# Kernel tuning notes

Hardware: AMD Instinct MI355X
Metric: run time of the kernel (lower is better)

The kernel has to match this reference:

```python
import jax, jax.numpy as jnp
import numpy as np

HEADS = 8
ALPHA = 0.2  # leaky relu negative slope


def setup_inputs() -> dict:
    key = jax.random.key(0)
    k1, k2, k3 = jax.random.split(key, 3)
    B, S, IN, H, F = 8, 1024, 768, HEADS, 64
    node_features = jax.random.normal(k1, (B, S, IN), dtype=jnp.float32)
    attention_mask = jnp.ones((B, S), dtype=jnp.int32)
    W = jax.random.normal(k2, (IN, H * F), dtype=jnp.float32) * 0.02
    a = jax.random.normal(k3, (2 * F,), dtype=jnp.float32) * 0.02
    return {"node_features": node_features, "attention_mask": attention_mask, "W": W, "a": a}


def reference(node_features, attention_mask, W, a):
    B, S, _ = node_features.shape
    H = HEADS
    F = W.shape[1] // H
    # Wh: [B, S, H, F]
    Wh = (node_features @ W).reshape(B, S, H, F)
    # Additive score a([Wh_i || Wh_j]) decomposes exactly into src_i + dst_j
    a_src, a_dst = a[:F], a[F:]
    src = jnp.einsum('bshf,f->bsh', Wh, a_src)  # contribution of node i
    dst = jnp.einsum('bshf,f->bsh', Wh, a_dst)  # contribution of node j
    e = src[:, :, None, :] + dst[:, None, :, :]          # [B, i, j, H]
    e = jax.nn.leaky_relu(e, negative_slope=ALPHA)
    e = jnp.transpose(e, (0, 3, 1, 2))                   # [B, H, i, j]
    mask = attention_mask[:, None, None, :] == 0         # mask over j
    e = jnp.where(mask, -jnp.inf, e)
    attn = jax.nn.softmax(e, axis=-1)                    # [B, H, S, S]
    # weighted sum over neighbors j: [B, i, H, F]
    h_prime = jnp.einsum('bhij,bjhf->bihf', attn, Wh)
    return h_prime.reshape(B, S, H * F)
```

## Files before the change

kernel.cpp:

```cpp
#include <hip/hip_runtime.h>
#include <math.h>


typedef __attribute__((ext_vector_type(8))) short short8;
typedef __attribute__((ext_vector_type(4))) float floatx4;

union Frag { short8 s8; uint4 u4; };

__device__ inline unsigned as_u(float f) { union { float f; unsigned u; } v; v.f = f; return v.u; }
__device__ inline float as_f(unsigned u) { union { unsigned u; float f; } v; v.u = u; return v.f; }

__device__ inline unsigned pk_rne(float a, float b) {
  unsigned ua = as_u(a); ua = ua + 0x7fffu + ((ua >> 16) & 1u);
  unsigned ub = as_u(b); ub = ub + 0x7fffu + ((ub >> 16) & 1u);
  return (ua >> 16) | (ub & 0xffff0000u);
}
__device__ inline unsigned short f2bf(float f) {
  unsigned u = as_u(f); u = u + 0x7fffu + ((u >> 16) & 1u);
  return (unsigned short)(u >> 16);
}

__global__ __launch_bounds__(256) void conv_w(const float* __restrict__ W,
                                              unsigned short* __restrict__ WbT) {
  __shared__ unsigned short tile[64][72];
  int kt = blockIdx.x >> 3, nt = blockIdx.x & 7;
  int k0 = kt * 64, n0 = nt * 64;
  int t = threadIdx.x;
  int kr = t >> 2, cs = (t & 3) * 16;
#pragma unroll
  for (int q = 0; q < 4; q++) {
    float4 v = *(const float4*)&W[(k0 + kr) * 512 + n0 + cs + q * 4];
    tile[cs + q * 4 + 0][kr] = f2bf(v.x);
    tile[cs + q * 4 + 1][kr] = f2bf(v.y);
    tile[cs + q * 4 + 2][kr] = f2bf(v.z);
    tile[cs + q * 4 + 3][kr] = f2bf(v.w);
  }
  __syncthreads();
  int nr = t >> 2, ks = (t & 3) * 16;
  uint4 d0 = *(const uint4*)&tile[nr][ks];
  uint4 d1 = *(const uint4*)&tile[nr][ks + 8];
  *(uint4*)&WbT[(n0 + nr) * 768 + k0 + ks] = d0;
  *(uint4*)&WbT[(n0 + nr) * 768 + k0 + ks + 8] = d1;
}

__global__ __launch_bounds__(256) void xconv(const float* __restrict__ X,
                                             unsigned short* __restrict__ Xb) {
  const int total = 8192 * 768 / 8;
  int stride = gridDim.x * 256;
  for (int i = blockIdx.x * 256 + threadIdx.x; i < total; i += stride) {
    float4 v0 = *(const float4*)&X[i * 8];
    float4 v1 = *(const float4*)&X[i * 8 + 4];
    uint4 o;
    o.x = pk_rne(v0.x, v0.y); o.y = pk_rne(v0.z, v0.w);
    o.z = pk_rne(v1.x, v1.y); o.w = pk_rne(v1.z, v1.w);
    *(uint4*)&Xb[i * 8] = o;
  }
}

__global__ __launch_bounds__(256) void gemm_xw(const unsigned short* __restrict__ Xb,
                                               const unsigned short* __restrict__ WbT,
                                               const float* __restrict__ a,
                                               const int* __restrict__ mask,
                                               unsigned short* __restrict__ WhT,
                                               float* __restrict__ srcT,
                                               float* __restrict__ dstT) {
  __shared__ unsigned short Asm[2][64 * 64];
  __shared__ unsigned short Bsm[2][64 * 64];
  __shared__ float sd[2][64], dd[2][64];
  int t = threadIdx.x, w = t >> 6, lane = t & 63;
  int quad = lane >> 4, l15 = lane & 15;
  int m0 = blockIdx.x * 64, n0 = blockIdx.y * 64;
  int wm = (w & 1) * 32, wn = (w >> 1) * 32;

  floatx4 acc[2][2];
#pragma unroll
  for (int mt = 0; mt < 2; mt++)
#pragma unroll
    for (int nt = 0; nt < 2; nt++)
#pragma unroll
      for (int r = 0; r < 4; r++) acc[mt][nt][r] = 0.f;

  int sf = t >> 3, skb = t & 7;
  int swz = (skb ^ (sf & 7)) * 8;
  const unsigned short* ga0 = &Xb[(m0 + sf) * 768 + skb * 8];
  const unsigned short* ga1 = &Xb[(m0 + sf + 32) * 768 + skb * 8];
  const unsigned short* gb0 = &WbT[(n0 + sf) * 768 + skb * 8];
  const unsigned short* gb1 = &WbT[(n0 + sf + 32) * 768 + skb * 8];

  int rdA0 = (wm + l15) * 64, rdA1 = (wm + 16 + l15) * 64;
  int keyA0 = (wm + l15) & 7, keyA1 = (wm + 16 + l15) & 7;
  int rdB0 = (wn + l15) * 64, rdB1 = (wn + 16 + l15) * 64;
  int keyB0 = (wn + l15) & 7, keyB1 = (wn + 16 + l15) & 7;

  uint4 av0 = *(const uint4*)&ga0[0];
  uint4 av1 = *(const uint4*)&ga1[0];
  uint4 bv0 = *(const uint4*)&gb0[0];
  uint4 bv1 = *(const uint4*)&gb1[0];

#pragma unroll 2
  for (int kc = 0; kc < 12; kc++) {
    unsigned short* bufA = &Asm[kc & 1][0];
    unsigned short* bufB = &Bsm[kc & 1][0];
    *(uint4*)&bufA[sf * 64 + swz] = av0;
    *(uint4*)&bufA[(sf + 32) * 64 + swz] = av1;
    *(uint4*)&bufB[sf * 64 + swz] = bv0;
    *(uint4*)&bufB[(sf + 32) * 64 + swz] = bv1;
    __syncthreads();
    if (kc < 11) {
      int off = (kc + 1) * 64;
      av0 = *(const uint4*)&ga0[off];
      av1 = *(const uint4*)&ga1[off];
      bv0 = *(const uint4*)&gb0[off];
      bv1 = *(const uint4*)&gb1[off];
    }
#pragma unroll
    for (int kc2 = 0; kc2 < 2; kc2++) {
      int kb = kc2 * 4 + quad;
      Frag fa0 = *(const Frag*)&bufA[rdA0 + ((kb ^ keyA0) * 8)];
      Frag fa1 = *(const Frag*)&bufA[rdA1 + ((kb ^ keyA1) * 8)];
      Frag fb0 = *(const Frag*)&bufB[rdB0 + ((kb ^ keyB0) * 8)];
      Frag fb1 = *(const Frag*)&bufB[rdB1 + ((kb ^ keyB1) * 8)];
      acc[0][0] = __builtin_amdgcn_mfma_f32_16x16x32_bf16(fa0.s8, fb0.s8, acc[0][0], 0, 0, 0);
      acc[0][1] = __builtin_amdgcn_mfma_f32_16x16x32_bf16(fa0.s8, fb1.s8, acc[0][1], 0, 0, 0);
      acc[1][0] = __builtin_amdgcn_mfma_f32_16x16x32_bf16(fa1.s8, fb0.s8, acc[1][0], 0, 0, 0);
      acc[1][1] = __builtin_amdgcn_mfma_f32_16x16x32_bf16(fa1.s8, fb1.s8, acc[1][1], 0, 0, 0);
    }
  }
  int h = n0 >> 6;
#pragma unroll
  for (int mt = 0; mt < 2; mt++) {
#pragma unroll
    for (int nt = 0; nt < 2; nt++) {
      int f = (wn + nt * 16 + l15) & 63;
      int m = m0 + wm + mt * 16 + quad * 4;
      int b = m >> 10, s = m & 1023;
      floatx4 cc = acc[mt][nt];
      uint2 st;
      st.x = pk_rne(cc[0], cc[1]);
      st.y = pk_rne(cc[2], cc[3]);
      *(uint2*)&WhT[((b * 8 + h) * 64 + f) * 1024 + s] = st;
    }
  }
  {
    float asv[2] = {a[wn + l15], a[wn + 16 + l15]};
    float adv[2] = {a[64 + wn + l15], a[64 + wn + 16 + l15]};
    float psrc[2][4], pdst[2][4];
#pragma unroll
    for (int mt = 0; mt < 2; mt++)
#pragma unroll
      for (int r = 0; r < 4; r++) {
        psrc[mt][r] = acc[mt][0][r] * asv[0] + acc[mt][1][r] * asv[1];
        pdst[mt][r] = acc[mt][0][r] * adv[0] + acc[mt][1][r] * adv[1];
      }
#pragma unroll
    for (int off = 1; off < 16; off <<= 1)
#pragma unroll
      for (int mt = 0; mt < 2; mt++)
#pragma unroll
        for (int r = 0; r < 4; r++) {
          psrc[mt][r] += __shfl_xor(psrc[mt][r], off);
          pdst[mt][r] += __shfl_xor(pdst[mt][r], off);
        }
    __syncthreads();
    if (l15 == 0) {
      int half = w >> 1;
#pragma unroll
      for (int mt = 0; mt < 2; mt++)
#pragma unroll
        for (int r = 0; r < 4; r++) {
          int m = wm + mt * 16 + quad * 4 + r;
          sd[half][m] = psrc[mt][r];
          dd[half][m] = pdst[mt][r];
        }
    }
    __syncthreads();
    if (t < 64) {
      int m = m0 + t;
      int b = m >> 10, s = m & 1023;
      float sv = sd[0][t] + sd[1][t];
      float dvv = dd[0][t] + dd[1][t];
      srcT[(b * 8 + h) * 1024 + s] = sv;
      dstT[(b * 8 + h) * 1024 + s] = mask[b * 1024 + s] ? dvv : -1e30f;
    }
  }
}

__global__ __launch_bounds__(256) void gat_attn(const unsigned short* __restrict__ WhT,
                                                const float* __restrict__ srcT,
                                                const float* __restrict__ dstT,
                                                float* __restrict__ out) {
  __shared__ unsigned short Bs[2][64 * 64];
  int t = threadIdx.x, w = t >> 6, lane = t & 63;
  int quad = lane >> 4, l15 = lane & 15;
  int bh = blockIdx.x, b = bh >> 3;
  int iw = blockIdx.y * 64 + w * 16;

  floatx4 acc[4], lacc;
#pragma unroll
  for (int ft = 0; ft < 4; ft++)
#pragma unroll
    for (int r = 0; r < 4; r++) acc[ft][r] = 0.f;
#pragma unroll
  for (int r = 0; r < 4; r++) lacc[r] = 0.f;

  float src_r = srcT[bh * 1024 + iw + l15];

  Frag ones;
  ones.u4.x = 0x3F803F80u; ones.u4.y = 0x3F803F80u;
  ones.u4.z = 0x3F803F80u; ones.u4.w = 0x3F803F80u;

  const unsigned short* Wg = WhT + bh * 64 * 1024;
  const float* dbase = &dstT[bh * 1024 + quad * 8];
  int sf0 = t >> 3, skb = t & 7;
  int swz = (skb ^ (sf0 & 7)) * 8;

  uint4 g0 = *(const uint4*)&Wg[sf0 * 1024 + skb * 8];
  uint4 g1 = *(const uint4*)&Wg[(sf0 + 32) * 1024 + skb * 8];
  float4 dv[4];
  dv[0] = *(const float4*)&dbase[0];
  dv[1] = *(const float4*)&dbase[4];
  dv[2] = *(const float4*)&dbase[32];
  dv[3] = *(const float4*)&dbase[36];

#pragma unroll 2
  for (int jt = 0; jt < 16; jt++) {
    int j0 = jt * 64;
    unsigned short* buf = &Bs[jt & 1][0];
    *(uint4*)&buf[sf0 * 64 + swz] = g0;
    *(uint4*)&buf[(sf0 + 32) * 64 + swz] = g1;
    __syncthreads();
    float4 ndv[4] = {dv[0], dv[1], dv[2], dv[3]};
    if (jt < 15) {
      g0 = *(const uint4*)&Wg[sf0 * 1024 + j0 + 64 + skb * 8];
      g1 = *(const uint4*)&Wg[(sf0 + 32) * 1024 + j0 + 64 + skb * 8];
      ndv[0] = *(const float4*)&dbase[j0 + 64];
      ndv[1] = *(const float4*)&dbase[j0 + 68];
      ndv[2] = *(const float4*)&dbase[j0 + 96];
      ndv[3] = *(const float4*)&dbase[j0 + 100];
    }
    Frag fragA[2];
#pragma unroll
    for (int jc = 0; jc < 2; jc++) {
      float dj[8] = {dv[jc * 2].x, dv[jc * 2].y, dv[jc * 2].z, dv[jc * 2].w,
                     dv[jc * 2 + 1].x, dv[jc * 2 + 1].y, dv[jc * 2 + 1].z, dv[jc * 2 + 1].w};
      unsigned pw[4];
#pragma unroll
      for (int pr = 0; pr < 4; pr++) {
        float x0 = src_r + dj[pr * 2];
        float x1 = src_r + dj[pr * 2 + 1];
        x0 = fmaxf(x0, 0.2f * x0);
        x1 = fmaxf(x1, 0.2f * x1);
        float p0 = __expf(x0), p1 = __expf(x1);
        pw[pr] = __builtin_amdgcn_perm(as_u(p1), as_u(p0), 0x07060302u);
      }
      fragA[jc].u4.x = pw[0];
      fragA[jc].u4.y = pw[1];
      fragA[jc].u4.z = pw[2];
      fragA[jc].u4.w = pw[3];
    }
#pragma unroll
    for (int jc = 0; jc < 2; jc++) {
      Frag fbr[4];
#pragma unroll
      for (int ft = 0; ft < 4; ft++) {
        int f = ft * 16 + l15;
        int kb = jc * 4 + quad;
        fbr[ft] = *(const Frag*)&buf[f * 64 + (kb ^ (f & 7)) * 8];
      }
#pragma unroll
      for (int ft = 0; ft < 4; ft++)
        acc[ft] = __builtin_amdgcn_mfma_f32_16x16x32_bf16(fragA[jc].s8, fbr[ft].s8,
                                                          acc[ft], 0, 0, 0);
      lacc = __builtin_amdgcn_mfma_f32_16x16x32_bf16(fragA[jc].s8, ones.s8, lacc, 0, 0, 0);
    }
#pragma unroll
    for (int q = 0; q < 4; q++) dv[q] = ndv[q];
  }
  float inv[4] = {1.f / lacc[0], 1.f / lacc[1], 1.f / lacc[2], 1.f / lacc[3]};
  int mrow = b * 1024 + iw + quad * 4;
#pragma unroll
  for (int ft = 0; ft < 4; ft++) {
    int col = (bh & 7) * 64 + ft * 16 + l15;
#pragma unroll
    for (int r = 0; r < 4; r++)
      out[(mrow + r) * 512 + col] = acc[ft][r] * inv[r];
  }
}

extern "C" void kernel_launch(void* const* d_in, const int* in_sizes, int n_in,
                              void* d_out, int out_size, void* d_ws, size_t ws_size,
                              hipStream_t stream) {
  const float* X = (const float*)d_in[0];
  const int* mask = (const int*)d_in[1];
  const float* W = (const float*)d_in[2];
  const float* a = (const float*)d_in[3];
  float* out = (float*)d_out;

  char* ws = (char*)d_ws;
  unsigned short* WhT = (unsigned short*)ws;
  unsigned short* WbT = (unsigned short*)(ws + 8388608);
  float* srcT = (float*)(ws + 9175040);
  float* dstT = (float*)(ws + 9437184);
  unsigned short* Xb = (unsigned short*)(ws + 9699328);

  conv_w<<<96, 256, 0, stream>>>(W, WbT);
  xconv<<<512, 256, 0, stream>>>(X, Xb);
  gemm_xw<<<dim3(128, 8), 256, 0, stream>>>(Xb, WbT, a, mask, WhT, srcT, dstT);
  gat_attn<<<dim3(64, 16), 256, 0, stream>>>(WhT, srcT, dstT, out);
}
```

Baseline: 116.6 us.

## Merge conversion kernels and use direct global-to-LDS loads with larger GEMM tiles

Fuses the weight and input bf16 conversion kernels into one launch to save a kernel launch. The projection GEMM now uses 128x64 tiles with 8 MFMA accumulators per wave, which raises reuse of each B fragment. It also replaces register-staged LDS stores with global_load_lds direct copies into a pre-swizzled layout, double-buffered with one barrier per k-step. The cost is more LDS and registers per block and half as many GEMM blocks, so fewer waves are resident to hide latency.

```diff
diff --git a/kernel.cpp b/kernel.cpp
--- a/kernel.cpp
+++ b/kernel.cpp
@@ -20,40 +20,47 @@
   return (unsigned short)(u >> 16);
 }
 
-__global__ __launch_bounds__(256) void conv_w(const float* __restrict__ W,
-                                              unsigned short* __restrict__ WbT) {
-  __shared__ unsigned short tile[64][72];
-  int kt = blockIdx.x >> 3, nt = blockIdx.x & 7;
-  int k0 = kt * 64, n0 = nt * 64;
+typedef __attribute__((address_space(3))) unsigned lds_u32;
+typedef const __attribute__((address_space(1))) unsigned glb_u32;
+__device__ inline void gload16(const void* g, void* l) {
+  __builtin_amdgcn_global_load_lds((glb_u32*)g, (lds_u32*)l, 16, 0, 0);
+}
+
+__global__ __launch_bounds__(256) void prep(const float* __restrict__ W,
+                                            unsigned short* __restrict__ WbT,
+                                            const float* __restrict__ X,
+                                            unsigned short* __restrict__ Xb) {
   int t = threadIdx.x;
-  int kr = t >> 2, cs = (t & 3) * 16;
-#pragma unroll
-  for (int q = 0; q < 4; q++) {
-    float4 v = *(const float4*)&W[(k0 + kr) * 512 + n0 + cs + q * 4];
-    tile[cs + q * 4 + 0][kr] = f2bf(v.x);
-    tile[cs + q * 4 + 1][kr] = f2bf(v.y);
-    tile[cs + q * 4 + 2][kr] = f2bf(v.z);
-    tile[cs + q * 4 + 3][kr] = f2bf(v.w);
-  }
-  __syncthreads();
-  int nr = t >> 2, ks = (t & 3) * 16;
-  uint4 d0 = *(const uint4*)&tile[nr][ks];
-  uint4 d1 = *(const uint4*)&tile[nr][ks + 8];
-  *(uint4*)&WbT[(n0 + nr) * 768 + k0 + ks] = d0;
-  *(uint4*)&WbT[(n0 + nr) * 768 + k0 + ks + 8] = d1;
-}
-
-__global__ __launch_bounds__(256) void xconv(const float* __restrict__ X,
-                                             unsigned short* __restrict__ Xb) {
-  const int total = 8192 * 768 / 8;
-  int stride = gridDim.x * 256;
-  for (int i = blockIdx.x * 256 + threadIdx.x; i < total; i += stride) {
-    float4 v0 = *(const float4*)&X[i * 8];
-    float4 v1 = *(const float4*)&X[i * 8 + 4];
-    uint4 o;
-    o.x = pk_rne(v0.x, v0.y); o.y = pk_rne(v0.z, v0.w);
-    o.z = pk_rne(v1.x, v1.y); o.w = pk_rne(v1.z, v1.w);
-    *(uint4*)&Xb[i * 8] = o;
+  if (blockIdx.x < 96) {
+    __shared__ unsigned short tile[64][72];
+    int kt = blockIdx.x >> 3, nt = blockIdx.x & 7;
+    int k0 = kt * 64, n0 = nt * 64;
+    int kr = t >> 2, cs = (t & 3) * 16;
+#pragma unroll
+    for (int q = 0; q < 4; q++) {
+      float4 v = *(const float4*)&W[(k0 + kr) * 512 + n0 + cs + q * 4];
+      tile[cs + q * 4 + 0][kr] = f2bf(v.x);
+      tile[cs + q * 4 + 1][kr] = f2bf(v.y);
+      tile[cs + q * 4 + 2][kr] = f2bf(v.z);
+      tile[cs + q * 4 + 3][kr] = f2bf(v.w);
+    }
+    __syncthreads();
+    int nr = t >> 2, ks = (t & 3) * 16;
+    uint4 d0 = *(const uint4*)&tile[nr][ks];
+    uint4 d1 = *(const uint4*)&tile[nr][ks + 8];
+    *(uint4*)&WbT[(n0 + nr) * 768 + k0 + ks] = d0;
+    *(uint4*)&WbT[(n0 + nr) * 768 + k0 + ks + 8] = d1;
+  } else {
+    const int total = 8192 * 768 / 8;
+    int stride = 512 * 256;
+    for (int i = (blockIdx.x - 96) * 256 + t; i < total; i += stride) {
+      float4 v0 = *(const float4*)&X[i * 8];
+      float4 v1 = *(const float4*)&X[i * 8 + 4];
+      uint4 o;
+      o.x = pk_rne(v0.x, v0.y); o.y = pk_rne(v0.z, v0.w);
+      o.z = pk_rne(v1.x, v1.y); o.w = pk_rne(v1.z, v1.w);
+      *(uint4*)&Xb[i * 8] = o;
+    }
   }
 }
 
@@ -64,74 +71,89 @@
                                                unsigned short* __restrict__ WhT,
                                                float* __restrict__ srcT,
                                                float* __restrict__ dstT) {
-  __shared__ unsigned short Asm[2][64 * 64];
+  __shared__ unsigned short Asm[2][128 * 64];
   __shared__ unsigned short Bsm[2][64 * 64];
-  __shared__ float sd[2][64], dd[2][64];
+  __shared__ float sd[2][128], dd[2][128];
   int t = threadIdx.x, w = t >> 6, lane = t & 63;
   int quad = lane >> 4, l15 = lane & 15;
-  int m0 = blockIdx.x * 64, n0 = blockIdx.y * 64;
-  int wm = (w & 1) * 32, wn = (w >> 1) * 32;
-
-  floatx4 acc[2][2];
-#pragma unroll
-  for (int mt = 0; mt < 2; mt++)
+  int m0 = blockIdx.x * 128, n0 = blockIdx.y * 64;
+  int wm = (w & 1) * 64, wn = (w >> 1) * 32;
+
+  floatx4 acc[4][2];
+#pragma unroll
+  for (int mt = 0; mt < 4; mt++)
 #pragma unroll
     for (int nt = 0; nt < 2; nt++)
 #pragma unroll
       for (int r = 0; r < 4; r++) acc[mt][nt][r] = 0.f;
 
-  int sf = t >> 3, skb = t & 7;
-  int swz = (skb ^ (sf & 7)) * 8;
-  const unsigned short* ga0 = &Xb[(m0 + sf) * 768 + skb * 8];
-  const unsigned short* ga1 = &Xb[(m0 + sf + 32) * 768 + skb * 8];
-  const unsigned short* gb0 = &WbT[(n0 + sf) * 768 + skb * 8];
-  const unsigned short* gb1 = &WbT[(n0 + sf + 32) * 768 + skb * 8];
-
-  int rdA0 = (wm + l15) * 64, rdA1 = (wm + 16 + l15) * 64;
-  int keyA0 = (wm + l15) & 7, keyA1 = (wm + 16 + l15) & 7;
-  int rdB0 = (wn + l15) * 64, rdB1 = (wn + 16 + l15) * 64;
-  int keyB0 = (wn + l15) & 7, keyB1 = (wn + 16 + l15) & 7;
-
-  uint4 av0 = *(const uint4*)&ga0[0];
-  uint4 av1 = *(const uint4*)&ga1[0];
-  uint4 bv0 = *(const uint4*)&gb0[0];
-  uint4 bv1 = *(const uint4*)&gb1[0];
+  int lr = lane >> 3;
+  int cb = (lane & 7) ^ lr;
+  const unsigned short* pa[4];
+  const unsigned short* pb[2];
+#pragma unroll
+  for (int i = 0; i < 4; i++)
+    pa[i] = &Xb[(m0 + w * 32 + i * 8 + lr) * 768 + cb * 8];
+#pragma unroll
+  for (int i = 0; i < 2; i++)
+    pb[i] = &WbT[(n0 + w * 16 + i * 8 + lr) * 768 + cb * 8];
+
+#define STAGE(bsel)                                                   \
+  do {                                                                \
+    unsigned short* dA = &Asm[bsel][w * 2048];                        \
+    unsigned short* dB = &Bsm[bsel][w * 1024];                        \
+    _Pragma("unroll") for (int i = 0; i < 4; i++) {                   \
+      gload16(pa[i], dA + i * 512);                                   \
+      pa[i] += 64;                                                    \
+    }                                                                 \
+    _Pragma("unroll") for (int i = 0; i < 2; i++) {                   \
+      gload16(pb[i], dB + i * 512);                                   \
+      pb[i] += 64;                                                    \
+    }                                                                 \
+  } while (0)
+
+  int key = l15 & 7;
+  int rA[4], rB[2];
+#pragma unroll
+  for (int mt = 0; mt < 4; mt++) rA[mt] = (wm + mt * 16 + l15) * 64;
+#pragma unroll
+  for (int nt = 0; nt < 2; nt++) rB[nt] = (wn + nt * 16 + l15) * 64;
+
+  STAGE(0);
+  __syncthreads();
 
 #pragma unroll 2
   for (int kc = 0; kc < 12; kc++) {
-    unsigned short* bufA = &Asm[kc & 1][0];
-    unsigned short* bufB = &Bsm[kc & 1][0];
-    *(uint4*)&bufA[sf * 64 + swz] = av0;
-    *(uint4*)&bufA[(sf + 32) * 64 + swz] = av1;
-    *(uint4*)&bufB[sf * 64 + swz] = bv0;
-    *(uint4*)&bufB[(sf + 32) * 64 + swz] = bv1;
-    __syncthreads();
-    if (kc < 11) {
-      int off = (kc + 1) * 64;
-      av0 = *(const uint4*)&ga0[off];
-      av1 = *(const uint4*)&ga1[off];
-      bv0 = *(const uint4*)&gb0[off];
-      bv1 = *(const uint4*)&gb1[off];
-    }
+    const int cur = kc & 1;
+    if (kc < 11) STAGE(cur ^ 1);
+    const unsigned short* bufA = &Asm[cur][0];
+    const unsigned short* bufB = &Bsm[cur][0];
 #pragma unroll
     for (int kc2 = 0; kc2 < 2; kc2++) {
       int kb = kc2 * 4 + quad;
-      Frag fa0 = *(const Frag*)&bufA[rdA0 + ((kb ^ keyA0) * 8)];
-      Frag fa1 = *(const Frag*)&bufA[rdA1 + ((kb ^ keyA1) * 8)];
-      Frag fb0 = *(const Frag*)&bufB[rdB0 + ((kb ^ keyB0) * 8)];
-      Frag fb1 = *(const Frag*)&bufB[rdB1 + ((kb ^ keyB1) * 8)];
-      acc[0][0] = __builtin_amdgcn_mfma_f32_16x16x32_bf16(fa0.s8, fb0.s8, acc[0][0], 0, 0, 0);
-      acc[0][1] = __builtin_amdgcn_mfma_f32_16x16x32_bf16(fa0.s8, fb1.s8, acc[0][1], 0, 0, 0);
-      acc[1][0] = __builtin_amdgcn_mfma_f32_16x16x32_bf16(fa1.s8, fb0.s8, acc[1][0], 0, 0, 0);
-      acc[1][1] = __builtin_amdgcn_mfma_f32_16x16x32_bf16(fa1.s8, fb1.s8, acc[1][1], 0, 0, 0);
-    }
-  }
+      int ko = (kb ^ key) * 8;
+      Frag fa[4], fb[2];
+#pragma unroll
+      for (int mt = 0; mt < 4; mt++) fa[mt] = *(const Frag*)&bufA[rA[mt] + ko];
+#pragma unroll
+      for (int nt = 0; nt < 2; nt++) fb[nt] = *(const Frag*)&bufB[rB[nt] + ko];
+#pragma unroll
+      for (int mt = 0; mt < 4; mt++)
+#pragma unroll
+        for (int nt = 0; nt < 2; nt++)
+          acc[mt][nt] = __builtin_amdgcn_mfma_f32_16x16x32_bf16(fa[mt].s8, fb[nt].s8,
+                                                                acc[mt][nt], 0, 0, 0);
+    }
+    __syncthreads();
+  }
+#undef STAGE
+
   int h = n0 >> 6;
 #pragma unroll
-  for (int mt = 0; mt < 2; mt++) {
+  for (int mt = 0; mt < 4; mt++) {
 #pragma unroll
     for (int nt = 0; nt < 2; nt++) {
-      int f = (wn + nt * 16 + l15) & 63;
+      int f = wn + nt * 16 + l15;
       int m = m0 + wm + mt * 16 + quad * 4;
       int b = m >> 10, s = m & 1023;
       floatx4 cc = acc[mt][nt];
@@ -144,9 +166,9 @@
   {
     float asv[2] = {a[wn + l15], a[wn + 16 + l15]};
     float adv[2] = {a[64 + wn + l15], a[64 + wn + 16 + l15]};
-    float psrc[2][4], pdst[2][4];
-#pragma unroll
-    for (int mt = 0; mt < 2; mt++)
+    float psrc[4][4], pdst[4][4];
+#pragma unroll
+    for (int mt = 0; mt < 4; mt++)
 #pragma unroll
       for (int r = 0; r < 4; r++) {
         psrc[mt][r] = acc[mt][0][r] * asv[0] + acc[mt][1][r] * asv[1];
@@ -155,17 +177,16 @@
 #pragma unroll
     for (int off = 1; off < 16; off <<= 1)
 #pragma unroll
-      for (int mt = 0; mt < 2; mt++)
+      for (int mt = 0; mt < 4; mt++)
 #pragma unroll
         for (int r = 0; r < 4; r++) {
           psrc[mt][r] += __shfl_xor(psrc[mt][r], off);
           pdst[mt][r] += __shfl_xor(pdst[mt][r], off);
         }
-    __syncthreads();
     if (l15 == 0) {
       int half = w >> 1;
 #pragma unroll
-      for (int mt = 0; mt < 2; mt++)
+      for (int mt = 0; mt < 4; mt++)
 #pragma unroll
         for (int r = 0; r < 4; r++) {
           int m = wm + mt * 16 + quad * 4 + r;
@@ -174,7 +195,7 @@
         }
     }
     __syncthreads();
-    if (t < 64) {
+    if (t < 128) {
       int m = m0 + t;
       int b = m >> 10, s = m & 1023;
       float sv = sd[0][t] + sd[1][t];
@@ -303,8 +324,7 @@
   float* dstT = (float*)(ws + 9437184);
   unsigned short* Xb = (unsigned short*)(ws + 9699328);
 
-  conv_w<<<96, 256, 0, stream>>>(W, WbT);
-  xconv<<<512, 256, 0, stream>>>(X, Xb);
-  gemm_xw<<<dim3(128, 8), 256, 0, stream>>>(Xb, WbT, a, mask, WhT, srcT, dstT);
+  prep<<<608, 256, 0, stream>>>(W, WbT, X, Xb);
+  gemm_xw<<<dim3(64, 8), 256, 0, stream>>>(Xb, WbT, a, mask, WhT, srcT, dstT);
   gat_attn<<<dim3(64, 16), 256, 0, stream>>>(WhT, srcT, dstT, out);
 }
```

After: 115.0 us. Within noise of the previous version (-1.4%).
